# Kernel tuning notes

Measured on AMD Instinct MI355X. Metric: run time of the kernel, lower is better.

The kernel has to match this reference:

```python
import jax, jax.numpy as jnp
import numpy as np

H = 32       # num query heads
KV = 8       # num kv heads
HD = 128     # head dim
G = H // KV  # groups


def setup_inputs() -> dict:
    key = jax.random.key(0)
    ks = jax.random.split(key, 7)
    B, S, P, D = 2, 2048, 1024, 4096
    s = 1.0 / np.sqrt(D)
    return {
        "x": jax.random.normal(ks[0], (B, S, D), jnp.float32),
        "past_k": jax.random.normal(ks[1], (B, P, KV, HD), jnp.float32),
        "past_v": jax.random.normal(ks[2], (B, P, KV, HD), jnp.float32),
        "Wq": jax.random.normal(ks[3], (D, H * HD), jnp.float32) * s,
        "Wk": jax.random.normal(ks[4], (D, KV * HD), jnp.float32) * s,
        "Wv": jax.random.normal(ks[5], (D, KV * HD), jnp.float32) * s,
        "Wo": jax.random.normal(ks[6], (D, D), jnp.float32) * s,
    }


def reference(x, past_k, past_v, Wq, Wk, Wv, Wo):
    B, S, D = x.shape
    q = (x @ Wq).reshape(B, S, H, HD)    # [B,S,H,hd]
    k = (x @ Wk).reshape(B, S, KV, HD)
    v = (x @ Wv).reshape(B, S, KV, HD)
    # KV-cache append (cache slice [:, :end])
    k_full = jnp.concatenate([past_k, k], axis=1)  # [B,T,KV,hd]
    v_full = jnp.concatenate([past_v, v], axis=1)
    T = k_full.shape[1]
    # repeat_interleave over head dim -> each kv head serves G query heads
    k_rep = jnp.repeat(k_full, G, axis=2)  # [B,T,H,hd]
    v_rep = jnp.repeat(v_full, G, axis=2)
    scale = 1.0 / np.sqrt(HD)
    scores = jnp.einsum('bshd,bthd->bhst', q, k_rep) * scale  # [B,H,S,T]
    # causal mask with cache offset: query i attends to j <= (T - S) + i
    allowed = (jnp.arange(S)[:, None] + (T - S)) >= jnp.arange(T)[None, :]
    scores = jnp.where(allowed[None, None], scores, jnp.float32(-jnp.inf))
    attn = jax.nn.softmax(scores, axis=-1)
    out = jnp.einsum('bhst,bthd->bshd', attn, v_rep).reshape(B, S, D)
    return out @ Wo
```

## Files before the change

kernel.cpp:

```cpp
#include <hip/hip_runtime.h>

typedef __bf16 bf16x8 __attribute__((ext_vector_type(8)));
typedef float f32x4 __attribute__((ext_vector_type(4)));

#define B_ 2
#define S_ 2048
#define D_ 4096
#define H_ 32
#define KV_ 8
#define G_ 4
#define HD_ 128
#define P_ 1024
#define T_ 3072

__device__ inline bf16x8 cvt8(const float4 a, const float4 b) {
  bf16x8 r;
  r[0] = (__bf16)a.x; r[1] = (__bf16)a.y; r[2] = (__bf16)a.z; r[3] = (__bf16)a.w;
  r[4] = (__bf16)b.x; r[5] = (__bf16)b.y; r[6] = (__bf16)b.z; r[7] = (__bf16)b.w;
  return r;
}

__global__ __launch_bounds__(256) void cvt_f32_bf16(const float* __restrict__ in,
                                                    __bf16* __restrict__ out) {
  const long i = ((long)blockIdx.x * 256 + threadIdx.x) * 8;
  float4 a = *(const float4*)(in + i);
  float4 b = *(const float4*)(in + i + 4);
  *(bf16x8*)(out + i) = cvt8(a, b);
}

__global__ __launch_bounds__(256) void transpose2d(const float* __restrict__ in,
                                                   __bf16* __restrict__ out,
                                                   int R, int C) {
  __shared__ float tl[32][33];
  const int tx = threadIdx.x, ty = threadIdx.y;
  const int c0 = blockIdx.x * 32, r0 = blockIdx.y * 32;
#pragma unroll
  for (int i = 0; i < 4; ++i)
    tl[ty + i * 8][tx] = in[(long)(r0 + ty + i * 8) * C + c0 + tx];
  __syncthreads();
#pragma unroll
  for (int i = 0; i < 4; ++i)
    out[(long)(c0 + ty + i * 8) * R + r0 + tx] = (__bf16)tl[tx][ty + i * 8];
}

__global__ __launch_bounds__(256) void build_vt(const float* __restrict__ past_v,
                                                const __bf16* __restrict__ vn,
                                                __bf16* __restrict__ vt) {
  __shared__ float tl[32][33];
  const int tx = threadIdx.x, ty = threadIdx.y;
  const int j0 = blockIdx.x * 32, hd0 = blockIdx.y * 32;
  const int b = blockIdx.z >> 3, kvh = blockIdx.z & 7;
#pragma unroll
  for (int i = 0; i < 4; ++i) {
    const int j = j0 + ty + i * 8;
    float val = (j < P_)
        ? past_v[((long)((b * P_ + j) * KV_ + kvh)) * HD_ + hd0 + tx]
        : (float)vn[((long)((b * S_ + (j - P_)) * KV_ + kvh)) * HD_ + hd0 + tx];
    tl[ty + i * 8][tx] = val;
  }
  __syncthreads();
#pragma unroll
  for (int i = 0; i < 4; ++i)
    vt[((long)((b * KV_ + kvh) * HD_ + hd0 + ty + i * 8)) * T_ + j0 + tx] =
        (__bf16)tl[tx][ty + i * 8];
}

template <typename OutT>
__global__ __launch_bounds__(256, 2) void gemm_bt(const __bf16* __restrict__ A,
                                                  const __bf16* __restrict__ Bt,
                                                  OutT* __restrict__ C,
                                                  int M, int N, int K) {
  __shared__ __align__(16) __bf16 As[128][40];
  __shared__ __align__(16) __bf16 Bs[128][40];
  const int t = threadIdx.x;
  const int lane = t & 63, wave = t >> 6;
  const int wm = (wave >> 1) * 64, wn = (wave & 1) * 64;
  const int l15 = lane & 15, quad = lane >> 4;
  const long m0 = (long)blockIdx.y * 128, n0 = (long)blockIdx.x * 128;

  const int srow = t >> 2;
  const int sc8 = (t & 3) * 8;
  const __bf16* Ap = A + (m0 + srow) * K + sc8;
  const __bf16* Bp = Bt + (n0 + srow) * K + sc8;
  const long rstep = (long)64 * K;

  f32x4 acc[4][4];
#pragma unroll
  for (int i = 0; i < 4; ++i)
#pragma unroll
    for (int j = 0; j < 4; ++j)
#pragma unroll
      for (int e = 0; e < 4; ++e) acc[i][j][e] = 0.0f;

  bf16x8 ra0 = *(const bf16x8*)(Ap);
  bf16x8 ra1 = *(const bf16x8*)(Ap + rstep);
  bf16x8 rb0 = *(const bf16x8*)(Bp);
  bf16x8 rb1 = *(const bf16x8*)(Bp + rstep);

  const int nk = K >> 5;
  for (int kt = 0; kt < nk; ++kt) {
    __syncthreads();
    *(bf16x8*)(&As[srow][sc8]) = ra0;
    *(bf16x8*)(&As[64 + srow][sc8]) = ra1;
    *(bf16x8*)(&Bs[srow][sc8]) = rb0;
    *(bf16x8*)(&Bs[64 + srow][sc8]) = rb1;
    if (kt + 1 < nk) {
      const __bf16* An = Ap + (kt + 1) * 32;
      const __bf16* Bn = Bp + (kt + 1) * 32;
      ra0 = *(const bf16x8*)(An);
      ra1 = *(const bf16x8*)(An + rstep);
      rb0 = *(const bf16x8*)(Bn);
      rb1 = *(const bf16x8*)(Bn + rstep);
    }
    __syncthreads();
    bf16x8 aF[4], bF[4];
#pragma unroll
    for (int i = 0; i < 4; ++i)
      aF[i] = *(const bf16x8*)(&As[wm + i * 16 + l15][quad * 8]);
#pragma unroll
    for (int i = 0; i < 4; ++i)
      bF[i] = *(const bf16x8*)(&Bs[wn + i * 16 + l15][quad * 8]);
#pragma unroll
    for (int i = 0; i < 4; ++i)
#pragma unroll
      for (int j = 0; j < 4; ++j)
        acc[i][j] = __builtin_amdgcn_mfma_f32_16x16x32_bf16(aF[i], bF[j],
                                                            acc[i][j], 0, 0, 0);
  }

#pragma unroll
  for (int i = 0; i < 4; ++i) {
    const long r0 = m0 + wm + i * 16 + quad * 4;
#pragma unroll
    for (int j = 0; j < 4; ++j) {
      const long col = n0 + wn + j * 16 + l15;
#pragma unroll
      for (int r = 0; r < 4; ++r)
        C[(r0 + r) * N + col] = (OutT)acc[i][j][r];
    }
  }
}

__global__ __launch_bounds__(256, 2) void attn_kernel(
    __bf16* qio,
    const float* __restrict__ pk,
    const __bf16* __restrict__ kn,
    const __bf16* __restrict__ vt) {
  __shared__ __align__(16) __bf16 Ks[32][136];
  __shared__ __align__(16) __bf16 Vs[128][40];
  __shared__ __align__(16) __bf16 Ps[4][16][40];
  const int t = threadIdx.x;
  const int lane = t & 63, w = t >> 6;
  const int l15 = lane & 15, quad = lane >> 4;
  const int s0 = blockIdx.x * 64;
  const int h = blockIdx.y;
  const int b = blockIdx.z;
  const int kvh = h >> 2;

  bf16x8 aQ[4];
  {
    const int qrow = s0 + w * 16 + l15;
    const __bf16* qp = qio + ((long)((b * S_ + qrow) * H_ + h)) * HD_ + quad * 8;
#pragma unroll
    for (int kt = 0; kt < 4; ++kt) aQ[kt] = *(const bf16x8*)(qp + kt * 32);
  }

  f32x4 O[8];
#pragma unroll
  for (int f = 0; f < 8; ++f)
#pragma unroll
    for (int e = 0; e < 4; ++e) O[f][e] = 0.0f;
  float m_r[4], l_r[4];
#pragma unroll
  for (int r = 0; r < 4; ++r) { m_r[r] = -__builtin_inff(); l_r[r] = 0.0f; }

  const float C2 = 1.4426950408889634f * 0.08838834764831845f;
  const int ntiles = (P_ + s0 + 63) / 32 + 1;

  for (int tile = 0; tile < ntiles; ++tile) {
    const int j0 = tile * 32;
    __syncthreads();
#pragma unroll
    for (int p = 0; p < 2; ++p) {
      const int li = p * 256 + t;
      const int key = li >> 4, ch = (li & 15) * 8;
      const int j = j0 + key;
      bf16x8 kv;
      if (j < P_) {
        const float* src = pk + ((long)((b * P_ + j) * KV_ + kvh)) * HD_ + ch;
        kv = cvt8(*(const float4*)src, *(const float4*)(src + 4));
      } else {
        kv = *(const bf16x8*)(kn + ((long)((b * S_ + (j - P_)) * KV_ + kvh)) * HD_ + ch);
      }
      *(bf16x8*)(&Ks[key][ch]) = kv;
    }
#pragma unroll
    for (int p = 0; p < 2; ++p) {
      const int li = p * 256 + t;
      const int hd = li >> 2, k8 = (li & 3) * 8;
      *(bf16x8*)(&Vs[hd][k8]) =
          *(const bf16x8*)(vt + ((long)((b * KV_ + kvh) * HD_ + hd)) * T_ + j0 + k8);
    }
    __syncthreads();

    f32x4 sc0, sc1;
#pragma unroll
    for (int e = 0; e < 4; ++e) { sc0[e] = 0.0f; sc1[e] = 0.0f; }
#pragma unroll
    for (int kt = 0; kt < 4; ++kt) {
      bf16x8 bk0 = *(const bf16x8*)(&Ks[l15][kt * 32 + quad * 8]);
      bf16x8 bk1 = *(const bf16x8*)(&Ks[16 + l15][kt * 32 + quad * 8]);
      sc0 = __builtin_amdgcn_mfma_f32_16x16x32_bf16(aQ[kt], bk0, sc0, 0, 0, 0);
      sc1 = __builtin_amdgcn_mfma_f32_16x16x32_bf16(aQ[kt], bk1, sc1, 0, 0, 0);
    }

    float alpha[4];
#pragma unroll
    for (int r = 0; r < 4; ++r) {
      const int bound = P_ + s0 + w * 16 + quad * 4 + r;
      float v0 = (j0 + l15 <= bound) ? sc0[r] : -__builtin_inff();
      float v1 = (j0 + 16 + l15 <= bound) ? sc1[r] : -__builtin_inff();
      float mt = fmaxf(v0, v1);
      mt = fmaxf(mt, __shfl_xor(mt, 1));
      mt = fmaxf(mt, __shfl_xor(mt, 2));
      mt = fmaxf(mt, __shfl_xor(mt, 4));
      mt = fmaxf(mt, __shfl_xor(mt, 8));
      const float mn = fmaxf(m_r[r], mt);
      const float p0 = exp2f((v0 - mn) * C2);
      const float p1 = exp2f((v1 - mn) * C2);
      float rs = p0 + p1;
      rs += __shfl_xor(rs, 1);
      rs += __shfl_xor(rs, 2);
      rs += __shfl_xor(rs, 4);
      rs += __shfl_xor(rs, 8);
      alpha[r] = exp2f((m_r[r] - mn) * C2);
      m_r[r] = mn;
      l_r[r] = l_r[r] * alpha[r] + rs;
      Ps[w][quad * 4 + r][l15] = (__bf16)p0;
      Ps[w][quad * 4 + r][16 + l15] = (__bf16)p1;
    }
#pragma unroll
    for (int f = 0; f < 8; ++f)
#pragma unroll
      for (int r = 0; r < 4; ++r) O[f][r] *= alpha[r];

    __syncthreads();

    bf16x8 aP = *(const bf16x8*)(&Ps[w][l15][quad * 8]);
#pragma unroll
    for (int f = 0; f < 8; ++f) {
      bf16x8 bV = *(const bf16x8*)(&Vs[f * 16 + l15][quad * 8]);
      O[f] = __builtin_amdgcn_mfma_f32_16x16x32_bf16(aP, bV, O[f], 0, 0, 0);
    }
  }

#pragma unroll
  for (int r = 0; r < 4; ++r) {
    const float inv = 1.0f / l_r[r];
    const long row = (long)((b * S_ + s0 + w * 16 + quad * 4 + r) * H_ + h);
#pragma unroll
    for (int f = 0; f < 8; ++f)
      qio[row * HD_ + f * 16 + l15] = (__bf16)(O[f][r] * inv);
  }
}

extern "C" void kernel_launch(void* const* d_in, const int* in_sizes, int n_in,
                              void* d_out, int out_size, void* d_ws, size_t ws_size,
                              hipStream_t stream) {
  const float* x  = (const float*)d_in[0];
  const float* pk = (const float*)d_in[1];
  const float* pv = (const float*)d_in[2];
  const float* Wq = (const float*)d_in[3];
  const float* Wk = (const float*)d_in[4];
  const float* Wv = (const float*)d_in[5];
  const float* Wo = (const float*)d_in[6];
  float* out = (float*)d_out;
  char* ws = (char*)d_ws;
  __bf16* wt = (__bf16*)(ws);
  __bf16* q  = (__bf16*)(ws + (size_t)33554432);
  __bf16* kn = (__bf16*)(ws + (size_t)67108864);
  __bf16* vn = (__bf16*)(ws + (size_t)75497472);
  __bf16* xb = (__bf16*)(ws + (size_t)83886080);
  __bf16* vt = (__bf16*)(ws + (size_t)83886080);

  dim3 tb(32, 8);
  cvt_f32_bf16<<<8192, 256, 0, stream>>>(x, xb);
  transpose2d<<<dim3(128, 128), tb, 0, stream>>>(Wq, wt, D_, D_);
  gemm_bt<__bf16><<<dim3(32, 32), 256, 0, stream>>>(xb, wt, q, B_ * S_, D_, D_);
  transpose2d<<<dim3(32, 128), tb, 0, stream>>>(Wk, wt, D_, KV_ * HD_);
  gemm_bt<__bf16><<<dim3(8, 32), 256, 0, stream>>>(xb, wt, kn, B_ * S_, KV_ * HD_, D_);
  transpose2d<<<dim3(32, 128), tb, 0, stream>>>(Wv, wt, D_, KV_ * HD_);
  gemm_bt<__bf16><<<dim3(8, 32), 256, 0, stream>>>(xb, wt, vn, B_ * S_, KV_ * HD_, D_);
  build_vt<<<dim3(96, 4, 16), tb, 0, stream>>>(pv, vn, vt);
  attn_kernel<<<dim3(32, 32, 2), 256, 0, stream>>>(q, pk, kn, vt);
  transpose2d<<<dim3(128, 128), tb, 0, stream>>>(Wo, wt, D_, D_);
  gemm_bt<float><<<dim3(32, 32), 256, 0, stream>>>(q, wt, out, B_ * S_, D_, D_);
}
```

Before: 1.309 ms.

## Use direct global-to-LDS loads in GEMM and enlarge attention tiles

The GEMM now loads tiles straight into LDS with global_load_lds instead of staging them through registers, drops the LDS row padding and raises launch bounds to three blocks per CU. The attention kernel processes 128 query rows per block (32 per wave) over 64-key tiles, skips fully masked tiles per wave and applies the causal mask only on diagonal tiles. It computes softmax row sums with an MFMA against a ones vector instead of shuffle reductions, and drops the block-wide barrier before the PV matmul. The GEMM change gives up register prefetch overlap and may bring LDS bank conflicts from the unpadded layout. The larger attention tiles raise register and LDS use, which may lower occupancy.

Measured after the change: 1.209 ms. -7.6%, faster.

```diff
diff --git a/kernel.cpp b/kernel.cpp
--- a/kernel.cpp
+++ b/kernel.cpp
@@ -2,6 +2,8 @@
 
 typedef __bf16 bf16x8 __attribute__((ext_vector_type(8)));
 typedef float f32x4 __attribute__((ext_vector_type(4)));
+using gptr_t = const __attribute__((address_space(1))) void*;
+using sptr_t = __attribute__((address_space(3))) void*;
 
 #define B_ 2
 #define S_ 2048
@@ -66,23 +68,27 @@
 }
 
 template <typename OutT>
-__global__ __launch_bounds__(256, 2) void gemm_bt(const __bf16* __restrict__ A,
+__global__ __launch_bounds__(256, 3) void gemm_bt(const __bf16* __restrict__ A,
                                                   const __bf16* __restrict__ Bt,
                                                   OutT* __restrict__ C,
                                                   int M, int N, int K) {
-  __shared__ __align__(16) __bf16 As[128][40];
-  __shared__ __align__(16) __bf16 Bs[128][40];
+  __shared__ __align__(16) __bf16 As[128][32];
+  __shared__ __align__(16) __bf16 Bs[128][32];
   const int t = threadIdx.x;
   const int lane = t & 63, wave = t >> 6;
   const int wm = (wave >> 1) * 64, wn = (wave & 1) * 64;
   const int l15 = lane & 15, quad = lane >> 4;
   const long m0 = (long)blockIdx.y * 128, n0 = (long)blockIdx.x * 128;
 
-  const int srow = t >> 2;
-  const int sc8 = (t & 3) * 8;
-  const __bf16* Ap = A + (m0 + srow) * K + sc8;
-  const __bf16* Bp = Bt + (n0 + srow) * K + sc8;
-  const long rstep = (long)64 * K;
+  const int srow = wave * 32 + (lane >> 2);
+  const int scol = (lane & 3) * 8;
+  const __bf16* Ap = A + (m0 + srow) * K + scol;
+  const __bf16* Bp = Bt + (n0 + srow) * K + scol;
+  const long rstep = 16L * K;
+  sptr_t ldsA0 = (sptr_t)&As[wave * 32][0];
+  sptr_t ldsA1 = (sptr_t)&As[wave * 32 + 16][0];
+  sptr_t ldsB0 = (sptr_t)&Bs[wave * 32][0];
+  sptr_t ldsB1 = (sptr_t)&Bs[wave * 32 + 16][0];
 
   f32x4 acc[4][4];
 #pragma unroll
@@ -91,27 +97,14 @@
     for (int j = 0; j < 4; ++j)
 #pragma unroll
       for (int e = 0; e < 4; ++e) acc[i][j][e] = 0.0f;
-
-  bf16x8 ra0 = *(const bf16x8*)(Ap);
-  bf16x8 ra1 = *(const bf16x8*)(Ap + rstep);
-  bf16x8 rb0 = *(const bf16x8*)(Bp);
-  bf16x8 rb1 = *(const bf16x8*)(Bp + rstep);
 
   const int nk = K >> 5;
   for (int kt = 0; kt < nk; ++kt) {
     __syncthreads();
-    *(bf16x8*)(&As[srow][sc8]) = ra0;
-    *(bf16x8*)(&As[64 + srow][sc8]) = ra1;
-    *(bf16x8*)(&Bs[srow][sc8]) = rb0;
-    *(bf16x8*)(&Bs[64 + srow][sc8]) = rb1;
-    if (kt + 1 < nk) {
-      const __bf16* An = Ap + (kt + 1) * 32;
-      const __bf16* Bn = Bp + (kt + 1) * 32;
-      ra0 = *(const bf16x8*)(An);
-      ra1 = *(const bf16x8*)(An + rstep);
-      rb0 = *(const bf16x8*)(Bn);
-      rb1 = *(const bf16x8*)(Bn + rstep);
-    }
+    __builtin_amdgcn_global_load_lds((gptr_t)(Ap + kt * 32), ldsA0, 16, 0, 0);
+    __builtin_amdgcn_global_load_lds((gptr_t)(Ap + rstep + kt * 32), ldsA1, 16, 0, 0);
+    __builtin_amdgcn_global_load_lds((gptr_t)(Bp + kt * 32), ldsB0, 16, 0, 0);
+    __builtin_amdgcn_global_load_lds((gptr_t)(Bp + rstep + kt * 32), ldsB1, 16, 0, 0);
     __syncthreads();
     bf16x8 aF[4], bF[4];
 #pragma unroll
@@ -146,42 +139,52 @@
     const float* __restrict__ pk,
     const __bf16* __restrict__ kn,
     const __bf16* __restrict__ vt) {
-  __shared__ __align__(16) __bf16 Ks[32][136];
-  __shared__ __align__(16) __bf16 Vs[128][40];
-  __shared__ __align__(16) __bf16 Ps[4][16][40];
+  __shared__ __align__(16) __bf16 Ks[64][136];
+  __shared__ __align__(16) __bf16 Vs[128][72];
+  __shared__ __align__(16) __bf16 Ps[4][32][72];
   const int t = threadIdx.x;
   const int lane = t & 63, w = t >> 6;
   const int l15 = lane & 15, quad = lane >> 4;
-  const int s0 = blockIdx.x * 64;
-  const int h = blockIdx.y;
-  const int b = blockIdx.z;
+  const int s0 = blockIdx.x * 128;
+  const int h = blockIdx.y, b = blockIdx.z;
   const int kvh = h >> 2;
 
-  bf16x8 aQ[4];
-  {
-    const int qrow = s0 + w * 16 + l15;
+  bf16x8 aQ[2][4];
+#pragma unroll
+  for (int mi = 0; mi < 2; ++mi) {
+    const int qrow = s0 + w * 32 + mi * 16 + l15;
     const __bf16* qp = qio + ((long)((b * S_ + qrow) * H_ + h)) * HD_ + quad * 8;
 #pragma unroll
-    for (int kt = 0; kt < 4; ++kt) aQ[kt] = *(const bf16x8*)(qp + kt * 32);
-  }
-
-  f32x4 O[8];
-#pragma unroll
-  for (int f = 0; f < 8; ++f)
-#pragma unroll
-    for (int e = 0; e < 4; ++e) O[f][e] = 0.0f;
-  float m_r[4], l_r[4];
-#pragma unroll
-  for (int r = 0; r < 4; ++r) { m_r[r] = -__builtin_inff(); l_r[r] = 0.0f; }
+    for (int kt = 0; kt < 4; ++kt) aQ[mi][kt] = *(const bf16x8*)(qp + kt * 32);
+  }
+
+  f32x4 O[2][8];
+#pragma unroll
+  for (int mi = 0; mi < 2; ++mi)
+#pragma unroll
+    for (int f = 0; f < 8; ++f)
+#pragma unroll
+      for (int e = 0; e < 4; ++e) O[mi][f][e] = 0.0f;
+  float m_r[2][4], l_r[2][4];
+#pragma unroll
+  for (int mi = 0; mi < 2; ++mi)
+#pragma unroll
+    for (int r = 0; r < 4; ++r) { m_r[mi][r] = -__builtin_inff(); l_r[mi][r] = 0.0f; }
+
+  bf16x8 ones;
+#pragma unroll
+  for (int e = 0; e < 8; ++e) ones[e] = (__bf16)1.0f;
 
   const float C2 = 1.4426950408889634f * 0.08838834764831845f;
-  const int ntiles = (P_ + s0 + 63) / 32 + 1;
+  const int ntiles = (P_ + s0 + 128) / 64;
+  const int wave_last_key = P_ + s0 + w * 32 + 31;
+  const int wave_min_bound = P_ + s0 + w * 32;
 
   for (int tile = 0; tile < ntiles; ++tile) {
-    const int j0 = tile * 32;
+    const int j0 = tile * 64;
     __syncthreads();
 #pragma unroll
-    for (int p = 0; p < 2; ++p) {
+    for (int p = 0; p < 4; ++p) {
       const int li = p * 256 + t;
       const int key = li >> 4, ch = (li & 15) * 8;
       const int j = j0 + key;
@@ -195,72 +198,108 @@
       *(bf16x8*)(&Ks[key][ch]) = kv;
     }
 #pragma unroll
-    for (int p = 0; p < 2; ++p) {
+    for (int p = 0; p < 4; ++p) {
       const int li = p * 256 + t;
-      const int hd = li >> 2, k8 = (li & 3) * 8;
+      const int hd = li >> 3, k8 = (li & 7) * 8;
       *(bf16x8*)(&Vs[hd][k8]) =
           *(const bf16x8*)(vt + ((long)((b * KV_ + kvh) * HD_ + hd)) * T_ + j0 + k8);
     }
     __syncthreads();
 
-    f32x4 sc0, sc1;
-#pragma unroll
-    for (int e = 0; e < 4; ++e) { sc0[e] = 0.0f; sc1[e] = 0.0f; }
-#pragma unroll
-    for (int kt = 0; kt < 4; ++kt) {
-      bf16x8 bk0 = *(const bf16x8*)(&Ks[l15][kt * 32 + quad * 8]);
-      bf16x8 bk1 = *(const bf16x8*)(&Ks[16 + l15][kt * 32 + quad * 8]);
-      sc0 = __builtin_amdgcn_mfma_f32_16x16x32_bf16(aQ[kt], bk0, sc0, 0, 0, 0);
-      sc1 = __builtin_amdgcn_mfma_f32_16x16x32_bf16(aQ[kt], bk1, sc1, 0, 0, 0);
-    }
-
-    float alpha[4];
+    if (j0 > wave_last_key) continue;
+
+    f32x4 sc[2][4];
+#pragma unroll
+    for (int mi = 0; mi < 2; ++mi)
+#pragma unroll
+      for (int kf = 0; kf < 4; ++kf)
+#pragma unroll
+        for (int e = 0; e < 4; ++e) sc[mi][kf][e] = 0.0f;
+#pragma unroll
+    for (int kf = 0; kf < 4; ++kf) {
+#pragma unroll
+      for (int kt = 0; kt < 4; ++kt) {
+        bf16x8 bk = *(const bf16x8*)(&Ks[kf * 16 + l15][kt * 32 + quad * 8]);
+        sc[0][kf] = __builtin_amdgcn_mfma_f32_16x16x32_bf16(aQ[0][kt], bk, sc[0][kf], 0, 0, 0);
+        sc[1][kf] = __builtin_amdgcn_mfma_f32_16x16x32_bf16(aQ[1][kt], bk, sc[1][kf], 0, 0, 0);
+      }
+    }
+
+    const bool need_mask = (j0 + 63 > wave_min_bound);
+    float alpha[2][4];
+#pragma unroll
+    for (int mi = 0; mi < 2; ++mi) {
+#pragma unroll
+      for (int r = 0; r < 4; ++r) {
+        float v0 = sc[mi][0][r], v1 = sc[mi][1][r];
+        float v2 = sc[mi][2][r], v3 = sc[mi][3][r];
+        if (need_mask) {
+          const int bound = P_ + s0 + w * 32 + mi * 16 + quad * 4 + r;
+          v0 = (j0 + l15 <= bound) ? v0 : -__builtin_inff();
+          v1 = (j0 + 16 + l15 <= bound) ? v1 : -__builtin_inff();
+          v2 = (j0 + 32 + l15 <= bound) ? v2 : -__builtin_inff();
+          v3 = (j0 + 48 + l15 <= bound) ? v3 : -__builtin_inff();
+        }
+        float mt = fmaxf(fmaxf(v0, v1), fmaxf(v2, v3));
+        mt = fmaxf(mt, __shfl_xor(mt, 1));
+        mt = fmaxf(mt, __shfl_xor(mt, 2));
+        mt = fmaxf(mt, __shfl_xor(mt, 4));
+        mt = fmaxf(mt, __shfl_xor(mt, 8));
+        const float mn = fmaxf(m_r[mi][r], mt);
+        const float p0 = exp2f((v0 - mn) * C2);
+        const float p1 = exp2f((v1 - mn) * C2);
+        const float p2 = exp2f((v2 - mn) * C2);
+        const float p3 = exp2f((v3 - mn) * C2);
+        alpha[mi][r] = exp2f((m_r[mi][r] - mn) * C2);
+        m_r[mi][r] = mn;
+        const int row = mi * 16 + quad * 4 + r;
+        Ps[w][row][l15] = (__bf16)p0;
+        Ps[w][row][16 + l15] = (__bf16)p1;
+        Ps[w][row][32 + l15] = (__bf16)p2;
+        Ps[w][row][48 + l15] = (__bf16)p3;
+      }
+    }
+#pragma unroll
+    for (int mi = 0; mi < 2; ++mi)
+#pragma unroll
+      for (int f = 0; f < 8; ++f)
+#pragma unroll
+        for (int r = 0; r < 4; ++r) O[mi][f][r] *= alpha[mi][r];
+
+    f32x4 sums[2];
+#pragma unroll
+    for (int e = 0; e < 4; ++e) { sums[0][e] = 0.0f; sums[1][e] = 0.0f; }
+#pragma unroll
+    for (int kf2 = 0; kf2 < 2; ++kf2) {
+      bf16x8 aP0 = *(const bf16x8*)(&Ps[w][l15][kf2 * 32 + quad * 8]);
+      bf16x8 aP1 = *(const bf16x8*)(&Ps[w][16 + l15][kf2 * 32 + quad * 8]);
+      sums[0] = __builtin_amdgcn_mfma_f32_16x16x32_bf16(aP0, ones, sums[0], 0, 0, 0);
+      sums[1] = __builtin_amdgcn_mfma_f32_16x16x32_bf16(aP1, ones, sums[1], 0, 0, 0);
+#pragma unroll
+      for (int f = 0; f < 8; ++f) {
+        bf16x8 bV = *(const bf16x8*)(&Vs[f * 16 + l15][kf2 * 32 + quad * 8]);
+        O[0][f] = __builtin_amdgcn_mfma_f32_16x16x32_bf16(aP0, bV, O[0][f], 0, 0, 0);
+        O[1][f] = __builtin_amdgcn_mfma_f32_16x16x32_bf16(aP1, bV, O[1][f], 0, 0, 0);
+      }
+    }
+#pragma unroll
+    for (int mi = 0; mi < 2; ++mi)
+#pragma unroll
+      for (int r = 0; r < 4; ++r)
+        l_r[mi][r] = l_r[mi][r] * alpha[mi][r] + sums[mi][r];
+  }
+
+#pragma unroll
+  for (int mi = 0; mi < 2; ++mi) {
 #pragma unroll
     for (int r = 0; r < 4; ++r) {
-      const int bound = P_ + s0 + w * 16 + quad * 4 + r;
-      float v0 = (j0 + l15 <= bound) ? sc0[r] : -__builtin_inff();
-      float v1 = (j0 + 16 + l15 <= bound) ? sc1[r] : -__builtin_inff();
-      float mt = fmaxf(v0, v1);
-      mt = fmaxf(mt, __shfl_xor(mt, 1));
-      mt = fmaxf(mt, __shfl_xor(mt, 2));
-      mt = fmaxf(mt, __shfl_xor(mt, 4));
-      mt = fmaxf(mt, __shfl_xor(mt, 8));
-      const float mn = fmaxf(m_r[r], mt);
-      const float p0 = exp2f((v0 - mn) * C2);
-      const float p1 = exp2f((v1 - mn) * C2);
-      float rs = p0 + p1;
-      rs += __shfl_xor(rs, 1);
-      rs += __shfl_xor(rs, 2);
-      rs += __shfl_xor(rs, 4);
-      rs += __shfl_xor(rs, 8);
-      alpha[r] = exp2f((m_r[r] - mn) * C2);
-      m_r[r] = mn;
-      l_r[r] = l_r[r] * alpha[r] + rs;
-      Ps[w][quad * 4 + r][l15] = (__bf16)p0;
-      Ps[w][quad * 4 + r][16 + l15] = (__bf16)p1;
-    }
-#pragma unroll
-    for (int f = 0; f < 8; ++f)
-#pragma unroll
-      for (int r = 0; r < 4; ++r) O[f][r] *= alpha[r];
-
-    __syncthreads();
-
-    bf16x8 aP = *(const bf16x8*)(&Ps[w][l15][quad * 8]);
-#pragma unroll
-    for (int f = 0; f < 8; ++f) {
-      bf16x8 bV = *(const bf16x8*)(&Vs[f * 16 + l15][quad * 8]);
-      O[f] = __builtin_amdgcn_mfma_f32_16x16x32_bf16(aP, bV, O[f], 0, 0, 0);
-    }
-  }
-
-#pragma unroll
-  for (int r = 0; r < 4; ++r) {
-    const float inv = 1.0f / l_r[r];
-    const long row = (long)((b * S_ + s0 + w * 16 + quad * 4 + r) * H_ + h);
-#pragma unroll
-    for (int f = 0; f < 8; ++f)
-      qio[row * HD_ + f * 16 + l15] = (__bf16)(O[f][r] * inv);
+      const float inv = 1.0f / l_r[mi][r];
+      const long row =
+          (long)((b * S_ + s0 + w * 32 + mi * 16 + quad * 4 + r) * H_ + h);
+#pragma unroll
+      for (int f = 0; f < 8; ++f)
+        qio[row * HD_ + f * 16 + l15] = (__bf16)(O[mi][f][r] * inv);
+    }
   }
 }
 
@@ -292,7 +331,7 @@
   transpose2d<<<dim3(32, 128), tb, 0, stream>>>(Wv, wt, D_, KV_ * HD_);
   gemm_bt<__bf16><<<dim3(8, 32), 256, 0, stream>>>(xb, wt, vn, B_ * S_, KV_ * HD_, D_);
   build_vt<<<dim3(96, 4, 16), tb, 0, stream>>>(pv, vn, vt);
-  attn_kernel<<<dim3(32, 32, 2), 256, 0, stream>>>(q, pk, kn, vt);
+  attn_kernel<<<dim3(16, 32, 2), 256, 0, stream>>>(q, pk, kn, vt);
   transpose2d<<<dim3(128, 128), tb, 0, stream>>>(Wo, wt, D_, D_);
   gemm_bt<float><<<dim3(32, 32), 256, 0, stream>>>(q, wt, out, B_ * S_, D_, D_);
 }
```
